# Optimization experiments

Hardware: AMD Instinct MI355X
Metric: run time of the kernel (lower is better)

Reference implementation:

```python
import jax, jax.numpy as jnp
import numpy as np

GROUPS = 32
EPS = 1e-6
C = 512
HEADS = 8
B, N, K = 1, 2048, 128


def group_norm(x, w, b):
    # x: [B, C, N]
    Bx, Cx, Nx = x.shape
    xg = x.reshape(Bx, GROUPS, Cx // GROUPS, Nx)
    mu = xg.mean(axis=(2, 3), keepdims=True)
    var = xg.var(axis=(2, 3), keepdims=True)
    xn = ((xg - mu) / jnp.sqrt(var + EPS)).reshape(Bx, Cx, Nx)
    return xn * w[:, None] + b[:, None]


def conv1x1(h, w, b):
    # 1x1 Conv1d == per-position linear: w [out, in], h [B, in, N]
    return jnp.einsum('oc,bcn->bon', w, h) + b[:, None]


def setup_inputs() -> dict:
    key = jax.random.key(0)
    ks = jax.random.split(key, 8)
    x = jax.random.normal(ks[0], (B, C, N), dtype=jnp.float32)
    valid_indices_mask = jax.random.randint(ks[1], (N, K), 0, 2, dtype=jnp.int32)
    attendable_indices = jax.random.randint(ks[2], (N, K), 0, N, dtype=jnp.int32)
    s = 0.05
    return {
        'x': x,
        'valid_indices_mask': valid_indices_mask,
        'attendable_indices': attendable_indices,
        'gn_w': jnp.ones((C,), jnp.float32),
        'gn_b': jnp.zeros((C,), jnp.float32),
        'wq': jax.random.normal(ks[3], (C, C), jnp.float32) * s,
        'bq': jnp.zeros((C,), jnp.float32),
        'wk': jax.random.normal(ks[4], (C, C), jnp.float32) * s,
        'bk': jnp.zeros((C,), jnp.float32),
        'wv': jax.random.normal(ks[5], (C, C), jnp.float32) * s,
        'bv': jnp.zeros((C,), jnp.float32),
        'wp': jax.random.normal(ks[6], (C, C), jnp.float32) * s,
        'bp': jnp.zeros((C,), jnp.float32),
    }


def reference(x, valid_indices_mask, attendable_indices, gn_w, gn_b,
              wq, bq, wk, bk, wv, bv, wp, bp):
    b, c, n = x.shape
    d = c // HEADS
    h_ = group_norm(x, gn_w, gn_b)
    q = conv1x1(h_, wq, bq).reshape(b, HEADS, d, n)
    k = conv1x1(h_, wk, bk).reshape(b, HEADS, d, n)
    v = conv1x1(h_, wv, bv).reshape(b, HEADS, d, n)

    # gather per-query attendable keys/values: [b,h,n,d] indexed by [nq,K] -> [b,h,nq,K,d]
    kt = jnp.swapaxes(k, -1, -2)
    vt = jnp.swapaxes(v, -1, -2)
    ak = kt[:, :, attendable_indices]  # [b,h,nq,K,d]
    av = vt[:, :, attendable_indices]

    # beta = 1, no 1/sqrt(d) scaling in the sparse path (faithful to source)
    weights = jnp.einsum('bhqkd,bhdq->bhqk', ak, q)
    weights = jnp.where(valid_indices_mask[None, None] == 0, -jnp.inf, weights)
    weights = jax.nn.softmax(weights, axis=-1)

    o = jnp.einsum('bhqk,bhqkd->bhqd', weights, av)
    # permute(0,3,1,2).reshape(b,c,n): channel layout is d-major then head (as in source)
    o = jnp.transpose(o, (0, 3, 1, 2)).reshape(b, c, n)
    o = conv1x1(o, wp, bp)
    return x + o
```

## Files before the change

kernel.cpp:

```cpp
#include <hip/hip_runtime.h>
#include <hip/hip_bf16.h>
#include <math.h>

#define NPOS 2048
#define CH   512
#define KATT 128
#define NHEAD 8

typedef __attribute__((ext_vector_type(8))) short short8;
typedef __attribute__((ext_vector_type(4))) float f32x4;

static __device__ __forceinline__ ushort f2bf(float f) {
  union { float f; unsigned u; } v; v.f = f;
  unsigned r = (v.u + 0x7FFFu + ((v.u >> 16) & 1u)) >> 16;
  return (ushort)r;
}

static __device__ __forceinline__ void gl16(const void* g, void* l) {
  __builtin_amdgcn_global_load_lds(
      (const __attribute__((address_space(1))) unsigned int*)(uintptr_t)g,
      (__attribute__((address_space(3))) unsigned int*)(uintptr_t)l, 16, 0, 0);
}

__global__ __launch_bounds__(256) void gn1_k(const float* __restrict__ x,
                                             float* __restrict__ part) {
  const int b = blockIdx.x;
  const float* xp = x + (b >> 3) * 32768 + (b & 7) * 4096;
  float s = 0.f, ss = 0.f;
  for (int i = threadIdx.x; i < 4096; i += 256) {
    float v = xp[i];
    s += v;
    ss += v * v;
  }
  __shared__ float rs[256], rq[256];
  rs[threadIdx.x] = s;
  rq[threadIdx.x] = ss;
  __syncthreads();
  for (int off = 128; off > 0; off >>= 1) {
    if (threadIdx.x < (unsigned)off) {
      rs[threadIdx.x] += rs[threadIdx.x + off];
      rq[threadIdx.x] += rq[threadIdx.x + off];
    }
    __syncthreads();
  }
  if (threadIdx.x == 0) {
    part[b * 2] = rs[0];
    part[b * 2 + 1] = rq[0];
  }
}

__global__ __launch_bounds__(256) void gn2_k(const float* __restrict__ x,
    const float* __restrict__ part, const float* __restrict__ gw,
    const float* __restrict__ gb, ushort* __restrict__ ht) {
  const int g = blockIdx.x >> 4;
  const int chunk = blockIdx.x & 15;
  float s = 0.f, ss = 0.f;
#pragma unroll
  for (int o = 0; o < 8; ++o) {
    s += part[(g * 8 + o) * 2];
    ss += part[(g * 8 + o) * 2 + 1];
  }
  const float inv_n = 1.f / 32768.f;
  const float mu = s * inv_n;
  const float var = ss * inv_n - mu * mu;
  const float rstd = rsqrtf(var + 1e-6f);

  const int half = threadIdx.x >> 7;
  const int pos = chunk * 128 + (threadIdx.x & 127);
  unsigned pk[4];
#pragma unroll
  for (int c2 = 0; c2 < 4; ++c2) {
    unsigned p = 0;
#pragma unroll
    for (int e = 0; e < 2; ++e) {
      const int cc = half * 8 + c2 * 2 + e;
      const int ch = g * 16 + cc;
      const float a = gw[ch] * rstd;
      const float v = x[ch * NPOS + pos] * a + (gb[ch] - mu * a);
      p |= ((unsigned)f2bf(v)) << (16 * e);
    }
    pk[c2] = p;
  }
  *(uint4*)(ht + pos * CH + g * 16 + half * 8) = make_uint4(pk[0], pk[1], pk[2], pk[3]);
}

__global__ __launch_bounds__(256) void prep_k(const float* __restrict__ wq,
    const float* __restrict__ wk, const float* __restrict__ wv,
    const float* __restrict__ wp, const float* __restrict__ bq,
    const float* __restrict__ bk, const float* __restrict__ bv,
    ushort* __restrict__ wqkv, ushort* __restrict__ wppb,
    float* __restrict__ bqkv) {
  const int bid = blockIdx.x;
  if (bid < 768) {
    const int m = bid >> 8;
    const float* src = m == 0 ? wq : (m == 1 ? wk : wv);
    const int i = (bid & 255) * 1024 + threadIdx.x * 4;
    const float4 v = *(const float4*)(src + i);
    uint2 p;
    p.x = (unsigned)f2bf(v.x) | ((unsigned)f2bf(v.y) << 16);
    p.y = (unsigned)f2bf(v.z) | ((unsigned)f2bf(v.w) << 16);
    *(uint2*)(wqkv + m * 262144 + i) = p;
  } else if (bid < 896) {
    __shared__ float lds[2048];
    const int co0 = (bid - 768) * 4;
    for (int t = threadIdx.x; t < 2048; t += 256) lds[t] = wp[co0 * 512 + t];
    __syncthreads();
    ushort o8[8];
#pragma unroll
    for (int e = 0; e < 8; ++e) {
      const int jj = threadIdx.x * 8 + e;
      const int col = jj >> 9;
      const int sl = jj & 511;
      o8[e] = f2bf(lds[col * 512 + (sl & 63) * 8 + (sl >> 6)]);
    }
    *(uint4*)(wppb + co0 * 512 + threadIdx.x * 8) = *(uint4*)o8;
  } else {
    for (int i = threadIdx.x; i < 1536; i += 256)
      bqkv[i] = i < 512 ? bq[i] : (i < 1024 ? bk[i - 512] : bv[i - 1024]);
  }
}

template<int TM, int WN, int MODE>
__global__ __launch_bounds__(256) void mm_k(const ushort* __restrict__ A,
    const ushort* __restrict__ Bm, const float* __restrict__ bias,
    const float* __restrict__ resid, float* __restrict__ outF) {
  constexpr int WM = 4 / WN;
  constexpr int FM = TM / (WM * 16);
  constexpr int FN = 64 / (WN * 16);
  __shared__ ushort As[TM * 64];
  __shared__ ushort Bs[64 * 64];
  const int mBase = blockIdx.x * TM;
  const int nBase = blockIdx.y * 64;
  const int tid = threadIdx.x;
  const int l = tid & 63;
  const int w = tid >> 6;
  const int wm = w / WN, wn = w % WN;
  const int sub8 = l >> 3;
  const int c16 = (l & 7) << 4;
  f32x4 acc[FM][FN] = {};

  for (int k0 = 0; k0 < 512; k0 += 64) {
#pragma unroll
    for (int c = 0; c < TM / 32; ++c) {
      const int r0 = w * (TM / 4) + c * 8;
      const int row = r0 + sub8;
      const int sc = c16 ^ ((row & 7) << 4);
      gl16(A + (mBase + row) * 512 + k0 + (sc >> 1), (char*)As + r0 * 128);
    }
#pragma unroll
    for (int c = 0; c < 2; ++c) {
      const int r0 = w * 16 + c * 8;
      const int row = r0 + sub8;
      const int sc = c16 ^ ((row & 7) << 4);
      gl16(Bm + (nBase + row) * 512 + k0 + (sc >> 1), (char*)Bs + r0 * 128);
    }
    __syncthreads();
#pragma unroll
    for (int ks = 0; ks < 2; ++ks) {
      const int kb = ks * 64 + ((l >> 4) << 4);
      short8 afr[FM], bfr[FN];
#pragma unroll
      for (int fm = 0; fm < FM; ++fm) {
        const int ra = wm * (FM * 16) + fm * 16 + (l & 15);
        afr[fm] = *(const short8*)((const char*)As + ra * 128 + (kb ^ ((ra & 7) << 4)));
      }
#pragma unroll
      for (int fn = 0; fn < FN; ++fn) {
        const int rb = wn * (FN * 16) + fn * 16 + (l & 15);
        bfr[fn] = *(const short8*)((const char*)Bs + rb * 128 + (kb ^ ((rb & 7) << 4)));
      }
#pragma unroll
      for (int fm = 0; fm < FM; ++fm)
#pragma unroll
        for (int fn = 0; fn < FN; ++fn)
          acc[fm][fn] = __builtin_amdgcn_mfma_f32_16x16x32_bf16(afr[fm], bfr[fn], acc[fm][fn], 0, 0, 0);
    }
    __syncthreads();
  }

#pragma unroll
  for (int fm = 0; fm < FM; ++fm)
#pragma unroll
    for (int fn = 0; fn < FN; ++fn) {
      const int col = nBase + wn * (FN * 16) + fn * 16 + (l & 15);
#pragma unroll
      for (int r = 0; r < 4; ++r) {
        const int rowm = mBase + wm * (FM * 16) + fm * 16 + ((l >> 4) << 2) + r;
        if (MODE == 0) {
          const int off = (col >> 9) * (NPOS * CH) + rowm * CH + (col & 511);
          outF[off] = acc[fm][fn][r] + bias[col];
        } else {
          const int off = rowm * NPOS + col;
          outF[off] = acc[fm][fn][r] + bias[rowm] + resid[off];
        }
      }
    }
}

__global__ __launch_bounds__(256) void attn_k(const float* __restrict__ qt,
    const float* __restrict__ kt, const float* __restrict__ vt,
    const int* __restrict__ aidx, const int* __restrict__ vmask,
    ushort* __restrict__ ot) {
  __shared__ int ils[4][KATT];
  __shared__ float scs[4][KATT];
  __shared__ float prs[4][2 * KATT];
  const int w = threadIdx.x >> 6;
  const int lane = threadIdx.x & 63;
  const int p = blockIdx.x * 4 + w;
  const int hd = p & 7;
  const int qpos = p >> 3;
  const int quad = lane >> 2;
  const int sub = lane & 3;
  int* ils_w = ils[w];
  float* scs_w = scs[w];
  float* prs_w = prs[w];

  const float* qb = qt + qpos * CH + hd * 64;
  float4 qv[4];
#pragma unroll
  for (int t = 0; t < 4; ++t) qv[t] = *(const float4*)(qb + t * 16 + sub * 4);

  const int i0 = qpos * KATT + lane;
  const int idx0 = aidx[i0];
  const int idx1 = aidx[i0 + 64];
  const int m0 = vmask[i0];
  const int m1 = vmask[i0 + 64];

  const unsigned long long b0 = __ballot(m0 != 0);
  const unsigned long long b1 = __ballot(m1 != 0);
  const int nv0 = __popcll(b0);
  const int nv = nv0 + __popcll(b1);
  const unsigned long long low = (1ull << lane) - 1ull;
  ils_w[lane] = 0;
  ils_w[lane + 64] = 0;
  if (m0) ils_w[__popcll(b0 & low)] = idx0;
  if (m1) ils_w[nv0 + __popcll(b1 & low)] = idx1;

  for (int p8 = 0; p8 * 16 < nv; ++p8) {
    const int t = p8 * 16 + quad;
    const int ki = ils_w[t];
    const float* kr = kt + ki * CH + hd * 64;
    float s = 0.f;
#pragma unroll
    for (int tt = 0; tt < 4; ++tt) {
      const float4 kc = *(const float4*)(kr + tt * 16 + sub * 4);
      s += kc.x * qv[tt].x + kc.y * qv[tt].y + kc.z * qv[tt].z + kc.w * qv[tt].w;
    }
    s += __shfl_xor(s, 1);
    s += __shfl_xor(s, 2);
    if (sub == 0 && t < nv) scs_w[t] = s;
  }

  float s0 = (lane < nv) ? scs_w[lane] : -INFINITY;
  float s1 = (lane + 64 < nv) ? scs_w[lane + 64] : -INFINITY;
  float mx = fmaxf(s0, s1);
#pragma unroll
  for (int off = 32; off > 0; off >>= 1) mx = fmaxf(mx, __shfl_xor(mx, off));
  const float e0 = __expf(s0 - mx);
  const float e1 = __expf(s1 - mx);
  float lsum = (lane < nv ? e0 : 0.f) + (lane + 64 < nv ? e1 : 0.f);
#pragma unroll
  for (int off = 32; off > 0; off >>= 1) lsum += __shfl_xor(lsum, off);
  const float inv = 1.f / lsum;

  if (lane < nv) {
    prs_w[2 * lane] = e0 * inv;
    prs_w[2 * lane + 1] = __int_as_float(ils_w[lane]);
  }
  if (lane + 64 < nv) {
    prs_w[2 * (lane + 64)] = e1 * inv;
    prs_w[2 * (lane + 64) + 1] = __int_as_float(ils_w[lane + 64]);
  }

  const float* vb = vt + hd * 64 + lane;
  float o = 0.f;
  int kk = 0;
  for (; kk + 8 <= nv; kk += 8) {
    const float4 c0 = *(const float4*)&prs_w[2 * kk];
    const float4 c1 = *(const float4*)&prs_w[2 * kk + 4];
    const float4 c2 = *(const float4*)&prs_w[2 * kk + 8];
    const float4 c3 = *(const float4*)&prs_w[2 * kk + 12];
    float vv[8];
    vv[0] = vb[__float_as_int(c0.y) * CH];
    vv[1] = vb[__float_as_int(c0.w) * CH];
    vv[2] = vb[__float_as_int(c1.y) * CH];
    vv[3] = vb[__float_as_int(c1.w) * CH];
    vv[4] = vb[__float_as_int(c2.y) * CH];
    vv[5] = vb[__float_as_int(c2.w) * CH];
    vv[6] = vb[__float_as_int(c3.y) * CH];
    vv[7] = vb[__float_as_int(c3.w) * CH];
    o += c0.x * vv[0] + c0.z * vv[1] + c1.x * vv[2] + c1.z * vv[3] +
         c2.x * vv[4] + c2.z * vv[5] + c3.x * vv[6] + c3.z * vv[7];
  }
  for (; kk < nv; ++kk) {
    const float2 c = *(const float2*)&prs_w[2 * kk];
    o += c.x * vb[__float_as_int(c.y) * CH];
  }
  ot[qpos * CH + hd * 64 + lane] = f2bf(o);
}

extern "C" void kernel_launch(void* const* d_in, const int* in_sizes, int n_in,
                              void* d_out, int out_size, void* d_ws, size_t ws_size,
                              hipStream_t stream) {
  const float* x    = (const float*)d_in[0];
  const int* vmask  = (const int*)d_in[1];
  const int* aidx   = (const int*)d_in[2];
  const float* gnw  = (const float*)d_in[3];
  const float* gnb  = (const float*)d_in[4];
  const float* wq   = (const float*)d_in[5];
  const float* bq   = (const float*)d_in[6];
  const float* wk   = (const float*)d_in[7];
  const float* bk   = (const float*)d_in[8];
  const float* wv   = (const float*)d_in[9];
  const float* bv   = (const float*)d_in[10];
  const float* wp   = (const float*)d_in[11];
  const float* bp   = (const float*)d_in[12];
  float* out = (float*)d_out;

  char* ws = (char*)d_ws;
  ushort* ht    = (ushort*)(ws);
  float*  qt    = (float*)(ws + (2u  << 20));
  float*  kt    = (float*)(ws + (6u  << 20));
  float*  vt    = (float*)(ws + (10u << 20));
  ushort* ot    = (ushort*)(ws + (14u << 20));
  ushort* wqkv  = (ushort*)(ws + (16u << 20));
  ushort* wppb  = (ushort*)(ws + (17u << 20) + (512u << 10));
  float*  bqkv  = (float*)(ws + (18u << 20));
  float*  part  = (float*)(ws + (18u << 20) + (32u << 10));

  gn1_k<<<256, 256, 0, stream>>>(x, part);
  gn2_k<<<512, 256, 0, stream>>>(x, part, gnw, gnb, ht);
  prep_k<<<897, 256, 0, stream>>>(wq, wk, wv, wp, bq, bk, bv, wqkv, wppb, bqkv);

  mm_k<64, 2, 0><<<dim3(NPOS / 64, 1536 / 64), 256, 0, stream>>>(ht, wqkv, bqkv, nullptr, qt);

  attn_k<<<(NPOS * NHEAD) / 4, 256, 0, stream>>>(qt, kt, vt, aidx, vmask, ot);

  mm_k<32, 4, 1><<<dim3(CH / 32, NPOS / 64), 256, 0, stream>>>(wppb, ot, bp, x, out);
}
```

Measured before the change: 133.1 us.

## Merge GN stats into prep kernel, store V as bf16, batch K gathers

The group-norm statistics pass moves into the weight-prep kernel, saving one launch. The QKV GEMM now writes V as bf16, which halves the bytes of the random V gathers in attention. The score loop loads two K rows per iteration so more memory requests are in flight. V now carries bf16 rounding error into the output, and the score loop uses more registers.

```diff
diff --git a/kernel.cpp b/kernel.cpp
--- a/kernel.cpp
+++ b/kernel.cpp
@@ -15,6 +15,10 @@
   unsigned r = (v.u + 0x7FFFu + ((v.u >> 16) & 1u)) >> 16;
   return (ushort)r;
 }
+static __device__ __forceinline__ float bf2f(ushort u) {
+  union { unsigned u; float f; } v; v.u = ((unsigned)u) << 16;
+  return v.f;
+}
 
 static __device__ __forceinline__ void gl16(const void* g, void* l) {
   __builtin_amdgcn_global_load_lds(
@@ -22,30 +26,65 @@
       (__attribute__((address_space(3))) unsigned int*)(uintptr_t)l, 16, 0, 0);
 }
 
-__global__ __launch_bounds__(256) void gn1_k(const float* __restrict__ x,
-                                             float* __restrict__ part) {
-  const int b = blockIdx.x;
-  const float* xp = x + (b >> 3) * 32768 + (b & 7) * 4096;
-  float s = 0.f, ss = 0.f;
-  for (int i = threadIdx.x; i < 4096; i += 256) {
-    float v = xp[i];
-    s += v;
-    ss += v * v;
-  }
-  __shared__ float rs[256], rq[256];
-  rs[threadIdx.x] = s;
-  rq[threadIdx.x] = ss;
-  __syncthreads();
-  for (int off = 128; off > 0; off >>= 1) {
-    if (threadIdx.x < (unsigned)off) {
-      rs[threadIdx.x] += rs[threadIdx.x + off];
-      rq[threadIdx.x] += rq[threadIdx.x + off];
-    }
+__global__ __launch_bounds__(256) void prep_k(const float* __restrict__ x,
+    const float* __restrict__ wq, const float* __restrict__ wk,
+    const float* __restrict__ wv, const float* __restrict__ wp,
+    const float* __restrict__ bq, const float* __restrict__ bk,
+    const float* __restrict__ bv, float* __restrict__ part,
+    ushort* __restrict__ wqkv, ushort* __restrict__ wppb,
+    float* __restrict__ bqkv) {
+  const int bid = blockIdx.x;
+  if (bid < 256) {
+    const int b = bid;
+    const float* xp = x + (b >> 3) * 32768 + (b & 7) * 4096;
+    float s = 0.f, ss = 0.f;
+    for (int i = threadIdx.x; i < 4096; i += 256) {
+      float v = xp[i];
+      s += v;
+      ss += v * v;
+    }
+    __shared__ float rs[256], rq[256];
+    rs[threadIdx.x] = s;
+    rq[threadIdx.x] = ss;
     __syncthreads();
-  }
-  if (threadIdx.x == 0) {
-    part[b * 2] = rs[0];
-    part[b * 2 + 1] = rq[0];
+    for (int off = 128; off > 0; off >>= 1) {
+      if (threadIdx.x < (unsigned)off) {
+        rs[threadIdx.x] += rs[threadIdx.x + off];
+        rq[threadIdx.x] += rq[threadIdx.x + off];
+      }
+      __syncthreads();
+    }
+    if (threadIdx.x == 0) {
+      part[b * 2] = rs[0];
+      part[b * 2 + 1] = rq[0];
+    }
+  } else if (bid < 1024) {
+    const int wb = bid - 256;
+    const int m = wb >> 8;
+    const float* src = m == 0 ? wq : (m == 1 ? wk : wv);
+    const int i = (wb & 255) * 1024 + threadIdx.x * 4;
+    const float4 v = *(const float4*)(src + i);
+    uint2 p;
+    p.x = (unsigned)f2bf(v.x) | ((unsigned)f2bf(v.y) << 16);
+    p.y = (unsigned)f2bf(v.z) | ((unsigned)f2bf(v.w) << 16);
+    *(uint2*)(wqkv + m * 262144 + i) = p;
+  } else if (bid < 1152) {
+    __shared__ float lds[2048];
+    const int co0 = (bid - 1024) * 4;
+    for (int t = threadIdx.x; t < 2048; t += 256) lds[t] = wp[co0 * 512 + t];
+    __syncthreads();
+    ushort o8[8];
+#pragma unroll
+    for (int e = 0; e < 8; ++e) {
+      const int jj = threadIdx.x * 8 + e;
+      const int col = jj >> 9;
+      const int sl = jj & 511;
+      o8[e] = f2bf(lds[col * 512 + (sl & 63) * 8 + (sl >> 6)]);
+    }
+    *(uint4*)(wppb + co0 * 512 + threadIdx.x * 8) = *(uint4*)o8;
+  } else {
+    for (int i = threadIdx.x; i < 1536; i += 256)
+      bqkv[i] = i < 512 ? bq[i] : (i < 1024 ? bk[i - 512] : bv[i - 1024]);
   }
 }
 
@@ -84,46 +123,11 @@
   *(uint4*)(ht + pos * CH + g * 16 + half * 8) = make_uint4(pk[0], pk[1], pk[2], pk[3]);
 }
 
-__global__ __launch_bounds__(256) void prep_k(const float* __restrict__ wq,
-    const float* __restrict__ wk, const float* __restrict__ wv,
-    const float* __restrict__ wp, const float* __restrict__ bq,
-    const float* __restrict__ bk, const float* __restrict__ bv,
-    ushort* __restrict__ wqkv, ushort* __restrict__ wppb,
-    float* __restrict__ bqkv) {
-  const int bid = blockIdx.x;
-  if (bid < 768) {
-    const int m = bid >> 8;
-    const float* src = m == 0 ? wq : (m == 1 ? wk : wv);
-    const int i = (bid & 255) * 1024 + threadIdx.x * 4;
-    const float4 v = *(const float4*)(src + i);
-    uint2 p;
-    p.x = (unsigned)f2bf(v.x) | ((unsigned)f2bf(v.y) << 16);
-    p.y = (unsigned)f2bf(v.z) | ((unsigned)f2bf(v.w) << 16);
-    *(uint2*)(wqkv + m * 262144 + i) = p;
-  } else if (bid < 896) {
-    __shared__ float lds[2048];
-    const int co0 = (bid - 768) * 4;
-    for (int t = threadIdx.x; t < 2048; t += 256) lds[t] = wp[co0 * 512 + t];
-    __syncthreads();
-    ushort o8[8];
-#pragma unroll
-    for (int e = 0; e < 8; ++e) {
-      const int jj = threadIdx.x * 8 + e;
-      const int col = jj >> 9;
-      const int sl = jj & 511;
-      o8[e] = f2bf(lds[col * 512 + (sl & 63) * 8 + (sl >> 6)]);
-    }
-    *(uint4*)(wppb + co0 * 512 + threadIdx.x * 8) = *(uint4*)o8;
-  } else {
-    for (int i = threadIdx.x; i < 1536; i += 256)
-      bqkv[i] = i < 512 ? bq[i] : (i < 1024 ? bk[i - 512] : bv[i - 1024]);
-  }
-}
-
 template<int TM, int WN, int MODE>
 __global__ __launch_bounds__(256) void mm_k(const ushort* __restrict__ A,
     const ushort* __restrict__ Bm, const float* __restrict__ bias,
-    const float* __restrict__ resid, float* __restrict__ outF) {
+    const float* __restrict__ resid, float* __restrict__ outF,
+    ushort* __restrict__ outV) {
   constexpr int WM = 4 / WN;
   constexpr int FM = TM / (WM * 16);
   constexpr int FN = 64 / (WN * 16);
@@ -187,8 +191,12 @@
       for (int r = 0; r < 4; ++r) {
         const int rowm = mBase + wm * (FM * 16) + fm * 16 + ((l >> 4) << 2) + r;
         if (MODE == 0) {
-          const int off = (col >> 9) * (NPOS * CH) + rowm * CH + (col & 511);
-          outF[off] = acc[fm][fn][r] + bias[col];
+          const float v = acc[fm][fn][r] + bias[col];
+          if (col < 1024) {
+            outF[(col >> 9) * (NPOS * CH) + rowm * CH + (col & 511)] = v;
+          } else {
+            outV[rowm * CH + (col & 511)] = f2bf(v);
+          }
         } else {
           const int off = rowm * NPOS + col;
           outF[off] = acc[fm][fn][r] + bias[rowm] + resid[off];
@@ -198,7 +206,7 @@
 }
 
 __global__ __launch_bounds__(256) void attn_k(const float* __restrict__ qt,
-    const float* __restrict__ kt, const float* __restrict__ vt,
+    const float* __restrict__ kt, const ushort* __restrict__ vtb,
     const int* __restrict__ aidx, const int* __restrict__ vmask,
     ushort* __restrict__ ot) {
   __shared__ int ils[4][KATT];
@@ -236,19 +244,30 @@
   if (m0) ils_w[__popcll(b0 & low)] = idx0;
   if (m1) ils_w[nv0 + __popcll(b1 & low)] = idx1;
 
-  for (int p8 = 0; p8 * 16 < nv; ++p8) {
-    const int t = p8 * 16 + quad;
-    const int ki = ils_w[t];
-    const float* kr = kt + ki * CH + hd * 64;
-    float s = 0.f;
+  const int P = (nv + 15) >> 4;
+  for (int p8 = 0; p8 < P; p8 += 2) {
+    const int t0 = p8 * 16 + quad;
+    const int t1 = t0 + 16;
+    const bool has1 = (p8 + 1) < P;
+    const int ki0 = ils_w[t0];
+    const int ki1 = has1 ? ils_w[t1] : 0;
+    const float* kr0 = kt + ki0 * CH + hd * 64;
+    const float* kr1 = kt + ki1 * CH + hd * 64;
+    float4 kc0[4], kc1[4];
+#pragma unroll
+    for (int tt = 0; tt < 4; ++tt) kc0[tt] = *(const float4*)(kr0 + tt * 16 + sub * 4);
+#pragma unroll
+    for (int tt = 0; tt < 4; ++tt) kc1[tt] = *(const float4*)(kr1 + tt * 16 + sub * 4);
+    float s0 = 0.f, s1 = 0.f;
 #pragma unroll
     for (int tt = 0; tt < 4; ++tt) {
-      const float4 kc = *(const float4*)(kr + tt * 16 + sub * 4);
-      s += kc.x * qv[tt].x + kc.y * qv[tt].y + kc.z * qv[tt].z + kc.w * qv[tt].w;
-    }
-    s += __shfl_xor(s, 1);
-    s += __shfl_xor(s, 2);
-    if (sub == 0 && t < nv) scs_w[t] = s;
+      s0 += kc0[tt].x * qv[tt].x + kc0[tt].y * qv[tt].y + kc0[tt].z * qv[tt].z + kc0[tt].w * qv[tt].w;
+      s1 += kc1[tt].x * qv[tt].x + kc1[tt].y * qv[tt].y + kc1[tt].z * qv[tt].z + kc1[tt].w * qv[tt].w;
+    }
+    s0 += __shfl_xor(s0, 1); s0 += __shfl_xor(s0, 2);
+    s1 += __shfl_xor(s1, 1); s1 += __shfl_xor(s1, 2);
+    if (sub == 0 && t0 < nv) scs_w[t0] = s0;
+    if (sub == 0 && has1 && t1 < nv) scs_w[t1] = s1;
   }
 
   float s0 = (lane < nv) ? scs_w[lane] : -INFINITY;
@@ -272,7 +291,7 @@
     prs_w[2 * (lane + 64) + 1] = __int_as_float(ils_w[lane + 64]);
   }
 
-  const float* vb = vt + hd * 64 + lane;
+  const ushort* vb = vtb + hd * 64 + lane;
   float o = 0.f;
   int kk = 0;
   for (; kk + 8 <= nv; kk += 8) {
@@ -281,20 +300,20 @@
     const float4 c2 = *(const float4*)&prs_w[2 * kk + 8];
     const float4 c3 = *(const float4*)&prs_w[2 * kk + 12];
     float vv[8];
-    vv[0] = vb[__float_as_int(c0.y) * CH];
-    vv[1] = vb[__float_as_int(c0.w) * CH];
-    vv[2] = vb[__float_as_int(c1.y) * CH];
-    vv[3] = vb[__float_as_int(c1.w) * CH];
-    vv[4] = vb[__float_as_int(c2.y) * CH];
-    vv[5] = vb[__float_as_int(c2.w) * CH];
-    vv[6] = vb[__float_as_int(c3.y) * CH];
-    vv[7] = vb[__float_as_int(c3.w) * CH];
+    vv[0] = bf2f(vb[__float_as_int(c0.y) * CH]);
+    vv[1] = bf2f(vb[__float_as_int(c0.w) * CH]);
+    vv[2] = bf2f(vb[__float_as_int(c1.y) * CH]);
+    vv[3] = bf2f(vb[__float_as_int(c1.w) * CH]);
+    vv[4] = bf2f(vb[__float_as_int(c2.y) * CH]);
+    vv[5] = bf2f(vb[__float_as_int(c2.w) * CH]);
+    vv[6] = bf2f(vb[__float_as_int(c3.y) * CH]);
+    vv[7] = bf2f(vb[__float_as_int(c3.w) * CH]);
     o += c0.x * vv[0] + c0.z * vv[1] + c1.x * vv[2] + c1.z * vv[3] +
          c2.x * vv[4] + c2.z * vv[5] + c3.x * vv[6] + c3.z * vv[7];
   }
   for (; kk < nv; ++kk) {
     const float2 c = *(const float2*)&prs_w[2 * kk];
-    o += c.x * vb[__float_as_int(c.y) * CH];
+    o += c.x * bf2f(vb[__float_as_int(c.y) * CH]);
   }
   ot[qpos * CH + hd * 64 + lane] = f2bf(o);
 }
@@ -321,20 +340,22 @@
   ushort* ht    = (ushort*)(ws);
   float*  qt    = (float*)(ws + (2u  << 20));
   float*  kt    = (float*)(ws + (6u  << 20));
-  float*  vt    = (float*)(ws + (10u << 20));
+  ushort* vtb   = (ushort*)(ws + (10u << 20));
   ushort* ot    = (ushort*)(ws + (14u << 20));
   ushort* wqkv  = (ushort*)(ws + (16u << 20));
   ushort* wppb  = (ushort*)(ws + (17u << 20) + (512u << 10));
   float*  bqkv  = (float*)(ws + (18u << 20));
   float*  part  = (float*)(ws + (18u << 20) + (32u << 10));
 
-  gn1_k<<<256, 256, 0, stream>>>(x, part);
+  prep_k<<<1153, 256, 0, stream>>>(x, wq, wk, wv, wp, bq, bk, bv,
+                                   part, wqkv, wppb, bqkv);
   gn2_k<<<512, 256, 0, stream>>>(x, part, gnw, gnb, ht);
-  prep_k<<<897, 256, 0, stream>>>(wq, wk, wv, wp, bq, bk, bv, wqkv, wppb, bqkv);
-
-  mm_k<64, 2, 0><<<dim3(NPOS / 64, 1536 / 64), 256, 0, stream>>>(ht, wqkv, bqkv, nullptr, qt);
-
-  attn_k<<<(NPOS * NHEAD) / 4, 256, 0, stream>>>(qt, kt, vt, aidx, vmask, ot);
-
-  mm_k<32, 4, 1><<<dim3(CH / 32, NPOS / 64), 256, 0, stream>>>(wppb, ot, bp, x, out);
-}
+
+  mm_k<64, 2, 0><<<dim3(NPOS / 64, 1536 / 64), 256, 0, stream>>>(
+      ht, wqkv, bqkv, nullptr, qt, vtb);
+
+  attn_k<<<(NPOS * NHEAD) / 4, 256, 0, stream>>>(qt, kt, vtb, aidx, vmask, ot);
+
+  mm_k<32, 4, 1><<<dim3(CH / 32, NPOS / 64), 256, 0, stream>>>(
+      wppb, ot, bp, x, out, nullptr);
+}
```

Result: faster. 130.3 us (-2.1%).
